# Performance work log

Measured on AMD Instinct MI355X. Metric: run time of the kernel, lower is better.

## Reference

```python
import jax, jax.numpy as jnp
import numpy as np

B = 1024          # global batch
D = 512           # embedding_size
C = 100000        # num_classes (sum over 8 shards)
S = 64.0          # ArcFace scale
M = 0.5           # ArcFace additive angular margin
EPS = 1e-30


def setup_inputs() -> dict:
    key = jax.random.key(0)
    k1, k2, k3 = jax.random.split(key, 3)
    embeddings = jax.random.normal(k1, (B, D), dtype=jnp.float32)
    weight = jax.random.normal(k2, (C, D), dtype=jnp.float32)
    labels = jax.random.randint(k3, (B,), 0, C, dtype=jnp.int64)
    return {"embeddings": embeddings, "weight": weight, "labels": labels}


def reference(embeddings, weight, labels):
    # normalize(embeddings), normalize(weight) -> cosine logits
    ne = embeddings * jax.lax.rsqrt(jnp.sum(embeddings * embeddings, axis=1, keepdims=True))
    nw = weight * jax.lax.rsqrt(jnp.sum(weight * weight, axis=1, keepdims=True))
    logits = jnp.clip(jnp.einsum("bd,cd->bc", ne, nw), -1.0, 1.0)  # [B, C]

    rows = jnp.arange(B)
    target_logit = logits[rows, labels]
    # ArcFace: cos(theta + m), theta+m clipped to pi (insightface CombinedMarginLoss m2)
    theta = jnp.arccos(jnp.clip(target_logit, -1.0, 1.0))
    new_target = jnp.cos(jnp.minimum(theta + M, jnp.float32(np.pi)))
    logits = logits.at[rows, labels].set(new_target) * S

    # FusedDistCrossEntropy (single-device equivalent): stable softmax,
    # gather target prob, loss = -mean(log(clamp(p_target, 1e-30)))
    logp = jax.nn.log_softmax(logits, axis=1)
    p_target = jnp.exp(logp[rows, labels])
    loss = -jnp.mean(jnp.log(jnp.maximum(p_target, EPS)))
    return loss
```

## Files before the change

### kernel.cpp

```cpp
#include <hip/hip_runtime.h>
#include <hip/hip_bf16.h>
#include <math.h>
#include <stdint.h>

#define B_BATCH   1024
#define D_DIM     512
#define C_CLASSES 100000
#define BM        128
#define BN        128
#define BK        32
#define KITERS    (D_DIM / BK)
#define MTILES    (B_BATCH / BM)
#define NTILES    ((C_CLASSES + BN - 1) / BN)
#define NGROUPS   98
#define GRID_G    (8 * 8 * NGROUPS)
#define WBLK      (C_CLASSES / 8)
#define ABLK      (B_BATCH / 8)
#define LOG2E     1.44269504088896340736f
#define K64LOG2E  92.33248261689366f
#define COSM      0.87758256189037276f
#define SINM      0.47942553860420301f
#define NEG_LOG_EPS 69.07755278982137f

typedef short bf16x8 __attribute__((ext_vector_type(8)));
typedef float f32x4  __attribute__((ext_vector_type(4)));

static __device__ __forceinline__ unsigned short f2bf(float f) {
    unsigned int u = __builtin_bit_cast(unsigned int, f);
    u += 0x7fffu + ((u >> 16) & 1u);
    return (unsigned short)(u >> 16);
}

static __device__ __forceinline__ unsigned int pk_rne(float lo, float hi) {
    return (unsigned int)f2bf(lo) | ((unsigned int)f2bf(hi) << 16);
}

static __device__ __forceinline__ unsigned int pk_bf16_trunc(float lo, float hi) {
    return __builtin_amdgcn_perm(__builtin_bit_cast(unsigned int, hi),
                                 __builtin_bit_cast(unsigned int, lo),
                                 0x07060302u);
}

static __device__ __forceinline__ void gld16(const unsigned short* g, unsigned short* l) {
    __builtin_amdgcn_global_load_lds(
        (const __attribute__((address_space(1))) unsigned int*)g,
        (__attribute__((address_space(3))) unsigned int*)l, 16, 0, 0);
}

__global__ __launch_bounds__(256) void prep(const float* __restrict__ W,
                                            const float* __restrict__ E,
                                            unsigned short* __restrict__ Wbf,
                                            unsigned short* __restrict__ Abf,
                                            float* __restrict__ out) {
    const int blk  = blockIdx.x;
    const int wave = threadIdx.x >> 6;
    const int lane = threadIdx.x & 63;
    const bool isW = blk < WBLK;
    if (!isW && blk == WBLK && threadIdx.x == 0) *out = 0.f;

    const float* src = isW ? W : E;
    unsigned short* dst = isW ? Wbf : Abf;
    const int r0 = (isW ? blk : blk - WBLK) * 8 + wave * 2;
    const int r1 = r0 + 1;

    const float4* s0 = (const float4*)(src + (size_t)r0 * D_DIM);
    const float4* s1 = (const float4*)(src + (size_t)r1 * D_DIM);
    float4 a0 = s0[2 * lane], a1 = s0[2 * lane + 1];
    float4 b0 = s1[2 * lane], b1 = s1[2 * lane + 1];

    float sa = a0.x*a0.x + a0.y*a0.y + a0.z*a0.z + a0.w*a0.w
             + a1.x*a1.x + a1.y*a1.y + a1.z*a1.z + a1.w*a1.w;
    float sb = b0.x*b0.x + b0.y*b0.y + b0.z*b0.z + b0.w*b0.w
             + b1.x*b1.x + b1.y*b1.y + b1.z*b1.z + b1.w*b1.w;
    #pragma unroll
    for (int off = 1; off < 64; off <<= 1) {
        sa += __shfl_xor(sa, off);
        sb += __shfl_xor(sb, off);
    }
    float ia = rsqrtf(sa), ib = rsqrtf(sb);
    a0.x *= ia; a0.y *= ia; a0.z *= ia; a0.w *= ia;
    a1.x *= ia; a1.y *= ia; a1.z *= ia; a1.w *= ia;
    b0.x *= ib; b0.y *= ib; b0.z *= ib; b0.w *= ib;
    b1.x *= ib; b1.y *= ib; b1.z *= ib; b1.w *= ib;

    uint4 oa, ob;
    if (isW) {
        oa = (uint4){pk_bf16_trunc(a0.x, a0.y), pk_bf16_trunc(a0.z, a0.w),
                     pk_bf16_trunc(a1.x, a1.y), pk_bf16_trunc(a1.z, a1.w)};
        ob = (uint4){pk_bf16_trunc(b0.x, b0.y), pk_bf16_trunc(b0.z, b0.w),
                     pk_bf16_trunc(b1.x, b1.y), pk_bf16_trunc(b1.z, b1.w)};
    } else {
        oa = (uint4){pk_rne(a0.x, a0.y), pk_rne(a0.z, a0.w),
                     pk_rne(a1.x, a1.y), pk_rne(a1.z, a1.w)};
        ob = (uint4){pk_rne(b0.x, b0.y), pk_rne(b0.z, b0.w),
                     pk_rne(b1.x, b1.y), pk_rne(b1.z, b1.w)};
    }
    ((uint4*)(dst + (size_t)r0 * D_DIM))[lane] = oa;
    ((uint4*)(dst + (size_t)r1 * D_DIM))[lane] = ob;
}

template<bool EDGE>
static __device__ __forceinline__ float epi_term(float accv, int col, int lab,
                                                 float* __restrict__ st, int srow) {
    if (EDGE && col >= C_CLASSES) return 0.f;
    float t = exp2f(fminf(0.f, __builtin_fmaf(accv, K64LOG2E, -K64LOG2E)));
    if (col == lab) {
        float c = fminf(1.f, fmaxf(-1.f, accv));
        float sn = sqrtf(fmaxf(0.f, 1.f - c * c));
        float nm = c * COSM - sn * SINM;
        if (c < -COSM) nm = -1.f;
        float s = nm * 64.0f;
        st[srow] = s;
        t = exp2f((s - 64.0f) * LOG2E);
    }
    return t;
}

__global__ __launch_bounds__(256, 4) void gemm_cos(const unsigned short* __restrict__ Abf,
                                                   const unsigned short* __restrict__ Wbf,
                                                   const int* __restrict__ labels,
                                                   float* __restrict__ st,
                                                   float* __restrict__ partial) {
    __shared__ unsigned short As[BM * BK];
    __shared__ unsigned short Bs[BN * BK];
    __shared__ float rowSum[BM];
    __shared__ int   labs[BM];

    const int id = blockIdx.x;
    const int x  = id & 7;
    const int s  = id >> 3;
    const int mt = s & 7;
    const int y  = x + 8 * (s >> 3);
    if (y >= NTILES) return;
    const int m0 = mt * BM;
    const int n0 = y * BN;

    const int tid = threadIdx.x;
    if (tid < BM) { labs[tid] = labels[m0 + tid]; rowSum[tid] = 0.f; }

    const int lane = tid & 63;
    const int wave = tid >> 6;
    const int wm = wave & 1, wn = wave >> 1;
    const int l15 = lane & 15, quad = lane >> 4;

    const int rsub = lane >> 2;
    const int cg   = (lane & 3) * 8;
    const int c0 = wave * 2, c1 = wave * 2 + 1;
    const unsigned short* gA0 = Abf + (size_t)(m0 + c0 * 16 + rsub) * D_DIM + cg;
    const unsigned short* gA1 = Abf + (size_t)(m0 + c1 * 16 + rsub) * D_DIM + cg;
    const int bR0 = min(n0 + c0 * 16 + rsub, C_CLASSES - 1);
    const int bR1 = min(n0 + c1 * 16 + rsub, C_CLASSES - 1);
    const unsigned short* gB0 = Wbf + (size_t)bR0 * D_DIM + cg;
    const unsigned short* gB1 = Wbf + (size_t)bR1 * D_DIM + cg;
    unsigned short* lA0 = &As[c0 * 512];
    unsigned short* lA1 = &As[c1 * 512];
    unsigned short* lB0 = &Bs[c0 * 512];
    unsigned short* lB1 = &Bs[c1 * 512];

    const f32x4 z = (f32x4){0.f, 0.f, 0.f, 0.f};
    f32x4 a00 = z, a01 = z, a02 = z, a03 = z;
    f32x4 a10 = z, a11 = z, a12 = z, a13 = z;
    f32x4 a20 = z, a21 = z, a22 = z, a23 = z;
    f32x4 a30 = z, a31 = z, a32 = z, a33 = z;

    const int aro = (wm * 64 + l15) * BK + quad * 8;
    const int bro = (wn * 64 + l15) * BK + quad * 8;

    for (int kk = 0; kk < KITERS; ++kk) {
        __syncthreads();
        gld16(gA0, lA0); gld16(gA1, lA1);
        gld16(gB0, lB0); gld16(gB1, lB1);
        gA0 += BK; gA1 += BK; gB0 += BK; gB1 += BK;
        __syncthreads();

        bf16x8 af0 = *(const bf16x8*)&As[aro];
        bf16x8 af1 = *(const bf16x8*)&As[aro + 16 * BK];
        bf16x8 af2 = *(const bf16x8*)&As[aro + 32 * BK];
        bf16x8 af3 = *(const bf16x8*)&As[aro + 48 * BK];
        bf16x8 bf0 = *(const bf16x8*)&Bs[bro];
        bf16x8 bf1 = *(const bf16x8*)&Bs[bro + 16 * BK];
        bf16x8 bf2 = *(const bf16x8*)&Bs[bro + 32 * BK];
        bf16x8 bf3 = *(const bf16x8*)&Bs[bro + 48 * BK];

        a00 = __builtin_amdgcn_mfma_f32_16x16x32_bf16(af0, bf0, a00, 0, 0, 0);
        a01 = __builtin_amdgcn_mfma_f32_16x16x32_bf16(af0, bf1, a01, 0, 0, 0);
        a02 = __builtin_amdgcn_mfma_f32_16x16x32_bf16(af0, bf2, a02, 0, 0, 0);
        a03 = __builtin_amdgcn_mfma_f32_16x16x32_bf16(af0, bf3, a03, 0, 0, 0);
        a10 = __builtin_amdgcn_mfma_f32_16x16x32_bf16(af1, bf0, a10, 0, 0, 0);
        a11 = __builtin_amdgcn_mfma_f32_16x16x32_bf16(af1, bf1, a11, 0, 0, 0);
        a12 = __builtin_amdgcn_mfma_f32_16x16x32_bf16(af1, bf2, a12, 0, 0, 0);
        a13 = __builtin_amdgcn_mfma_f32_16x16x32_bf16(af1, bf3, a13, 0, 0, 0);
        a20 = __builtin_amdgcn_mfma_f32_16x16x32_bf16(af2, bf0, a20, 0, 0, 0);
        a21 = __builtin_amdgcn_mfma_f32_16x16x32_bf16(af2, bf1, a21, 0, 0, 0);
        a22 = __builtin_amdgcn_mfma_f32_16x16x32_bf16(af2, bf2, a22, 0, 0, 0);
        a23 = __builtin_amdgcn_mfma_f32_16x16x32_bf16(af2, bf3, a23, 0, 0, 0);
        a30 = __builtin_amdgcn_mfma_f32_16x16x32_bf16(af3, bf0, a30, 0, 0, 0);
        a31 = __builtin_amdgcn_mfma_f32_16x16x32_bf16(af3, bf1, a31, 0, 0, 0);
        a32 = __builtin_amdgcn_mfma_f32_16x16x32_bf16(af3, bf2, a32, 0, 0, 0);
        a33 = __builtin_amdgcn_mfma_f32_16x16x32_bf16(af3, bf3, a33, 0, 0, 0);
    }

    const int colbase = n0 + wn * 64 + l15;

    #define EPIROW(EDGE, A0, A1, A2, A3, MI)                                   \
    {                                                                          \
        _Pragma("unroll")                                                      \
        for (int r = 0; r < 4; ++r) {                                          \
            const int rloc = wm * 64 + (MI) * 16 + quad * 4 + r;               \
            const int lab = labs[rloc];                                        \
            float part = 0.f;                                                  \
            part += epi_term<EDGE>((A0)[r], colbase,      lab, st, m0 + rloc); \
            part += epi_term<EDGE>((A1)[r], colbase + 16, lab, st, m0 + rloc); \
            part += epi_term<EDGE>((A2)[r], colbase + 32, lab, st, m0 + rloc); \
            part += epi_term<EDGE>((A3)[r], colbase + 48, lab, st, m0 + rloc); \
            part += __shfl_xor(part, 1);                                       \
            part += __shfl_xor(part, 2);                                       \
            part += __shfl_xor(part, 4);                                       \
            part += __shfl_xor(part, 8);                                       \
            if (l15 == 0) atomicAdd(&rowSum[rloc], part);                      \
        }                                                                      \
    }

    if (n0 + BN <= C_CLASSES) {
        EPIROW(false, a00, a01, a02, a03, 0)
        EPIROW(false, a10, a11, a12, a13, 1)
        EPIROW(false, a20, a21, a22, a23, 2)
        EPIROW(false, a30, a31, a32, a33, 3)
    } else {
        EPIROW(true,  a00, a01, a02, a03, 0)
        EPIROW(true,  a10, a11, a12, a13, 1)
        EPIROW(true,  a20, a21, a22, a23, 2)
        EPIROW(true,  a30, a31, a32, a33, 3)
    }
    #undef EPIROW

    __syncthreads();
    if (tid < BM) partial[(size_t)(m0 + tid) * NTILES + y] = rowSum[tid];
}

__global__ __launch_bounds__(64) void reduce_loss(const float* __restrict__ partial,
                                                  const float* __restrict__ st,
                                                  float* __restrict__ out) {
    const int b = blockIdx.x;
    const int l = threadIdx.x;
    const float* row = partial + (size_t)b * NTILES;
    float L = 0.f;
    for (int t = l; t < NTILES; t += 64) L += row[t];
    #pragma unroll
    for (int off = 1; off < 64; off <<= 1) L += __shfl_xor(L, off);
    if (l == 0) {
        float logp = st[b] - 64.0f - logf(L);
        float lossb = fminf(-logp, NEG_LOG_EPS) * (1.0f / (float)B_BATCH);
        atomicAdd(out, lossb);
    }
}

extern "C" void kernel_launch(void* const* d_in, const int* in_sizes, int n_in,
                              void* d_out, int out_size, void* d_ws, size_t ws_size,
                              hipStream_t stream) {
    const float* emb = (const float*)d_in[0];
    const float* wgt = (const float*)d_in[1];
    const int*   lab = (const int*)d_in[2];
    float* out = (float*)d_out;
    char* ws = (char*)d_ws;

    const size_t WBF_B = (size_t)C_CLASSES * D_DIM * 2;
    const size_t ABF_B = (size_t)B_BATCH * D_DIM * 2;

    unsigned short* Wbf = (unsigned short*)ws;
    unsigned short* Abf = (unsigned short*)(ws + WBF_B);
    float* st      = (float*)(ws + WBF_B + ABF_B);
    float* partial = (float*)(ws + WBF_B + ABF_B + 4096);

    prep<<<WBLK + ABLK, 256, 0, stream>>>(wgt, emb, Wbf, Abf, out);
    gemm_cos<<<GRID_G, 256, 0, stream>>>(Abf, Wbf, lab, st, partial);
    reduce_loss<<<B_BATCH, 64, 0, stream>>>(partial, st, out);
}
```

Before: 451.2 us.

## Triple-buffer LDS tiles with async global-to-LDS prefetch in GEMM main loop

Replaces the single-buffered K loop, which had two barriers per step and no overlap, with a fully unrolled three-stage LDS ring. Global-to-LDS loads for step k+2 are issued while step k is computed, using explicit vmcnt waits and a single barrier per step. This aims to hide global load latency behind MFMA work. It triples the LDS footprint and lowers the launch-bounds occupancy hint from 4 to 3 blocks per CU.

```diff
diff --git a/kernel.cpp b/kernel.cpp
--- a/kernel.cpp
+++ b/kernel.cpp
@@ -10,7 +10,6 @@
 #define BN        128
 #define BK        32
 #define KITERS    (D_DIM / BK)
-#define MTILES    (B_BATCH / BM)
 #define NTILES    ((C_CLASSES + BN - 1) / BN)
 #define NGROUPS   98
 #define GRID_G    (8 * 8 * NGROUPS)
@@ -25,6 +24,9 @@
 typedef short bf16x8 __attribute__((ext_vector_type(8)));
 typedef float f32x4  __attribute__((ext_vector_type(4)));
 
+#define FENCE asm volatile("" ::: "memory")
+#define BAR() do { FENCE; __builtin_amdgcn_s_barrier(); FENCE; } while (0)
+
 static __device__ __forceinline__ unsigned short f2bf(float f) {
     unsigned int u = __builtin_bit_cast(unsigned int, f);
     u += 0x7fffu + ((u >> 16) & 1u);
@@ -41,7 +43,7 @@
                                  0x07060302u);
 }
 
-static __device__ __forceinline__ void gld16(const unsigned short* g, unsigned short* l) {
+static __device__ __forceinline__ void gld16(const unsigned short* g, const unsigned short* l) {
     __builtin_amdgcn_global_load_lds(
         (const __attribute__((address_space(1))) unsigned int*)g,
         (__attribute__((address_space(3))) unsigned int*)l, 16, 0, 0);
@@ -116,13 +118,13 @@
     return t;
 }
 
-__global__ __launch_bounds__(256, 4) void gemm_cos(const unsigned short* __restrict__ Abf,
+__global__ __launch_bounds__(256, 3) void gemm_cos(const unsigned short* __restrict__ Abf,
                                                    const unsigned short* __restrict__ Wbf,
                                                    const int* __restrict__ labels,
                                                    float* __restrict__ st,
                                                    float* __restrict__ partial) {
-    __shared__ unsigned short As[BM * BK];
-    __shared__ unsigned short Bs[BN * BK];
+    __shared__ unsigned short As[3][BM * BK];
+    __shared__ unsigned short Bs[3][BN * BK];
     __shared__ float rowSum[BM];
     __shared__ int   labs[BM];
 
@@ -137,6 +139,7 @@
 
     const int tid = threadIdx.x;
     if (tid < BM) { labs[tid] = labels[m0 + tid]; rowSum[tid] = 0.f; }
+    __syncthreads();
 
     const int lane = tid & 63;
     const int wave = tid >> 6;
@@ -152,10 +155,14 @@
     const int bR1 = min(n0 + c1 * 16 + rsub, C_CLASSES - 1);
     const unsigned short* gB0 = Wbf + (size_t)bR0 * D_DIM + cg;
     const unsigned short* gB1 = Wbf + (size_t)bR1 * D_DIM + cg;
-    unsigned short* lA0 = &As[c0 * 512];
-    unsigned short* lA1 = &As[c1 * 512];
-    unsigned short* lB0 = &Bs[c0 * 512];
-    unsigned short* lB1 = &Bs[c1 * 512];
+    const int lo0 = c0 * 512, lo1 = c1 * 512;
+
+    gld16(gA0, &As[0][lo0]); gld16(gA1, &As[0][lo1]);
+    gld16(gB0, &Bs[0][lo0]); gld16(gB1, &Bs[0][lo1]);
+    gA0 += BK; gA1 += BK; gB0 += BK; gB1 += BK;
+    gld16(gA0, &As[1][lo0]); gld16(gA1, &As[1][lo1]);
+    gld16(gB0, &Bs[1][lo0]); gld16(gB1, &Bs[1][lo1]);
+    gA0 += BK; gA1 += BK; gB0 += BK; gB1 += BK;
 
     const f32x4 z = (f32x4){0.f, 0.f, 0.f, 0.f};
     f32x4 a00 = z, a01 = z, a02 = z, a03 = z;
@@ -166,39 +173,58 @@
     const int aro = (wm * 64 + l15) * BK + quad * 8;
     const int bro = (wn * 64 + l15) * BK + quad * 8;
 
-    for (int kk = 0; kk < KITERS; ++kk) {
-        __syncthreads();
-        gld16(gA0, lA0); gld16(gA1, lA1);
-        gld16(gB0, lB0); gld16(gB1, lB1);
-        gA0 += BK; gA1 += BK; gB0 += BK; gB1 += BK;
-        __syncthreads();
-
-        bf16x8 af0 = *(const bf16x8*)&As[aro];
-        bf16x8 af1 = *(const bf16x8*)&As[aro + 16 * BK];
-        bf16x8 af2 = *(const bf16x8*)&As[aro + 32 * BK];
-        bf16x8 af3 = *(const bf16x8*)&As[aro + 48 * BK];
-        bf16x8 bf0 = *(const bf16x8*)&Bs[bro];
-        bf16x8 bf1 = *(const bf16x8*)&Bs[bro + 16 * BK];
-        bf16x8 bf2 = *(const bf16x8*)&Bs[bro + 32 * BK];
-        bf16x8 bf3 = *(const bf16x8*)&Bs[bro + 48 * BK];
-
-        a00 = __builtin_amdgcn_mfma_f32_16x16x32_bf16(af0, bf0, a00, 0, 0, 0);
-        a01 = __builtin_amdgcn_mfma_f32_16x16x32_bf16(af0, bf1, a01, 0, 0, 0);
-        a02 = __builtin_amdgcn_mfma_f32_16x16x32_bf16(af0, bf2, a02, 0, 0, 0);
-        a03 = __builtin_amdgcn_mfma_f32_16x16x32_bf16(af0, bf3, a03, 0, 0, 0);
-        a10 = __builtin_amdgcn_mfma_f32_16x16x32_bf16(af1, bf0, a10, 0, 0, 0);
-        a11 = __builtin_amdgcn_mfma_f32_16x16x32_bf16(af1, bf1, a11, 0, 0, 0);
-        a12 = __builtin_amdgcn_mfma_f32_16x16x32_bf16(af1, bf2, a12, 0, 0, 0);
-        a13 = __builtin_amdgcn_mfma_f32_16x16x32_bf16(af1, bf3, a13, 0, 0, 0);
-        a20 = __builtin_amdgcn_mfma_f32_16x16x32_bf16(af2, bf0, a20, 0, 0, 0);
-        a21 = __builtin_amdgcn_mfma_f32_16x16x32_bf16(af2, bf1, a21, 0, 0, 0);
-        a22 = __builtin_amdgcn_mfma_f32_16x16x32_bf16(af2, bf2, a22, 0, 0, 0);
-        a23 = __builtin_amdgcn_mfma_f32_16x16x32_bf16(af2, bf3, a23, 0, 0, 0);
-        a30 = __builtin_amdgcn_mfma_f32_16x16x32_bf16(af3, bf0, a30, 0, 0, 0);
-        a31 = __builtin_amdgcn_mfma_f32_16x16x32_bf16(af3, bf1, a31, 0, 0, 0);
-        a32 = __builtin_amdgcn_mfma_f32_16x16x32_bf16(af3, bf2, a32, 0, 0, 0);
-        a33 = __builtin_amdgcn_mfma_f32_16x16x32_bf16(af3, bf3, a33, 0, 0, 0);
-    }
+    #define KSTEP(T, CUR, STG, WAITN, DOSTAGE)                                 \
+    {                                                                          \
+        asm volatile("s_waitcnt vmcnt(" #WAITN ")" ::: "memory");              \
+        BAR();                                                                 \
+        if (DOSTAGE) {                                                         \
+            gld16(gA0, &As[STG][lo0]); gld16(gA1, &As[STG][lo1]);              \
+            gld16(gB0, &Bs[STG][lo0]); gld16(gB1, &Bs[STG][lo1]);              \
+            gA0 += BK; gA1 += BK; gB0 += BK; gB1 += BK;                        \
+        }                                                                      \
+        bf16x8 af0 = *(const bf16x8*)&As[CUR][aro];                            \
+        bf16x8 af1 = *(const bf16x8*)&As[CUR][aro + 16 * BK];                  \
+        bf16x8 af2 = *(const bf16x8*)&As[CUR][aro + 32 * BK];                  \
+        bf16x8 af3 = *(const bf16x8*)&As[CUR][aro + 48 * BK];                  \
+        bf16x8 bf0 = *(const bf16x8*)&Bs[CUR][bro];                            \
+        bf16x8 bf1 = *(const bf16x8*)&Bs[CUR][bro + 16 * BK];                  \
+        bf16x8 bf2 = *(const bf16x8*)&Bs[CUR][bro + 32 * BK];                  \
+        bf16x8 bf3 = *(const bf16x8*)&Bs[CUR][bro + 48 * BK];                  \
+        a00 = __builtin_amdgcn_mfma_f32_16x16x32_bf16(af0, bf0, a00, 0, 0, 0); \
+        a01 = __builtin_amdgcn_mfma_f32_16x16x32_bf16(af0, bf1, a01, 0, 0, 0); \
+        a02 = __builtin_amdgcn_mfma_f32_16x16x32_bf16(af0, bf2, a02, 0, 0, 0); \
+        a03 = __builtin_amdgcn_mfma_f32_16x16x32_bf16(af0, bf3, a03, 0, 0, 0); \
+        a10 = __builtin_amdgcn_mfma_f32_16x16x32_bf16(af1, bf0, a10, 0, 0, 0); \
+        a11 = __builtin_amdgcn_mfma_f32_16x16x32_bf16(af1, bf1, a11, 0, 0, 0); \
+        a12 = __builtin_amdgcn_mfma_f32_16x16x32_bf16(af1, bf2, a12, 0, 0, 0); \
+        a13 = __builtin_amdgcn_mfma_f32_16x16x32_bf16(af1, bf3, a13, 0, 0, 0); \
+        a20 = __builtin_amdgcn_mfma_f32_16x16x32_bf16(af2, bf0, a20, 0, 0, 0); \
+        a21 = __builtin_amdgcn_mfma_f32_16x16x32_bf16(af2, bf1, a21, 0, 0, 0); \
+        a22 = __builtin_amdgcn_mfma_f32_16x16x32_bf16(af2, bf2, a22, 0, 0, 0); \
+        a23 = __builtin_amdgcn_mfma_f32_16x16x32_bf16(af2, bf3, a23, 0, 0, 0); \
+        a30 = __builtin_amdgcn_mfma_f32_16x16x32_bf16(af3, bf0, a30, 0, 0, 0); \
+        a31 = __builtin_amdgcn_mfma_f32_16x16x32_bf16(af3, bf1, a31, 0, 0, 0); \
+        a32 = __builtin_amdgcn_mfma_f32_16x16x32_bf16(af3, bf2, a32, 0, 0, 0); \
+        a33 = __builtin_amdgcn_mfma_f32_16x16x32_bf16(af3, bf3, a33, 0, 0, 0); \
+    }
+
+    KSTEP(0,  0, 2, 4, true)
+    KSTEP(1,  1, 0, 4, true)
+    KSTEP(2,  2, 1, 4, true)
+    KSTEP(3,  0, 2, 4, true)
+    KSTEP(4,  1, 0, 4, true)
+    KSTEP(5,  2, 1, 4, true)
+    KSTEP(6,  0, 2, 4, true)
+    KSTEP(7,  1, 0, 4, true)
+    KSTEP(8,  2, 1, 4, true)
+    KSTEP(9,  0, 2, 4, true)
+    KSTEP(10, 1, 0, 4, true)
+    KSTEP(11, 2, 1, 4, true)
+    KSTEP(12, 0, 2, 4, true)
+    KSTEP(13, 1, 0, 4, true)
+    KSTEP(14, 2, 1, 4, false)
+    KSTEP(15, 0, 2, 0, false)
+    #undef KSTEP
 
     const int colbase = n0 + wn * 64 + l15;
 
```

After: 477.6 us. 1.06x slower.
